# Kernel optimization log

Measured on AMD Instinct MI355X. Metric: run time of the kernel, lower is better.

The kernel has to match this reference:

```python
import jax, jax.numpy as jnp
import numpy as np

NUM_HEADS = 16
KEY_SIZE = 64
VALUE_SIZE = 64
D_MODEL = 1024
B, S = 2, 2048

def setup_inputs() -> dict:
    key = jax.random.key(0)
    k1, k2 = jax.random.split(key)
    inputs = jax.random.normal(k1, (B, S, D_MODEL), dtype=jnp.float32)
    qkv_width = NUM_HEADS * (KEY_SIZE + KEY_SIZE + VALUE_SIZE)  # 3072
    W = jax.random.normal(k2, (D_MODEL, qkv_width), dtype=jnp.float32) / np.sqrt(D_MODEL)
    b = jnp.zeros((qkv_width,), dtype=jnp.float32)
    return {"inputs": inputs, "W": W, "b": b}

def reference(inputs, W, b):
    # Fused QKV projection: [B, S, H*(2k+v)]
    qkv = jnp.einsum("bsd,de->bse", inputs, W) + b
    Bsz, S_ = inputs.shape[0], inputs.shape[1]
    qkv = qkv.reshape(Bsz, S_, NUM_HEADS, 2 * KEY_SIZE + VALUE_SIZE)
    qkv = jnp.transpose(qkv, (0, 2, 1, 3))  # [B, H, S, 2k+v]
    q = qkv[..., :KEY_SIZE]
    k = qkv[..., KEY_SIZE:2 * KEY_SIZE]
    v = qkv[..., 2 * KEY_SIZE:]
    # NOTE: original multiplies by sqrt(key_size) (not divide) -- faithful.
    scores = jnp.einsum("bhqd,bhkd->bhqk", q, k) * jnp.sqrt(jnp.float32(KEY_SIZE))
    weights = jax.nn.softmax(scores, axis=-1)
    out = jnp.einsum("bhqk,bhkv->bhqv", weights, v)  # [B, H, S, v]
    out = jnp.transpose(out, (0, 2, 1, 3)).reshape(Bsz, S_, NUM_HEADS * VALUE_SIZE)
    return out
```

## Files before the change

### kernel.cpp

```cpp
#include <hip/hip_runtime.h>


#define S_LEN 2048
#define NH    16
#define DH    64
#define DM    1024
#define EW    3072
#define NROWS 4096
#define NT    32

#define QSCALE 11.5415603f

using f32x4 = __attribute__((ext_vector_type(4))) float;
using bf8   = __attribute__((ext_vector_type(8))) short;
using s4v   = __attribute__((ext_vector_type(4))) short;

static __device__ __forceinline__ short f2bf(float f) {
  union { float f; unsigned u; } a; a.f = f;
  unsigned r = a.u + 0x7fffu + ((a.u >> 16) & 1u);
  return (short)(r >> 16);
}
static __device__ __forceinline__ float bf2f(short h) {
  union { float f; unsigned u; } a;
  a.u = ((unsigned)(unsigned short)h) << 16;
  return a.f;
}
static __device__ __forceinline__ void gl16(const void* g, void* l) {
  __builtin_amdgcn_global_load_lds(
      (const __attribute__((address_space(1))) void*)g,
      (__attribute__((address_space(3))) void*)l, 16, 0, 0);
}

__global__ __launch_bounds__(256) void prep(
    const float* __restrict__ X, const float* __restrict__ W,
    short* __restrict__ Xh, short* __restrict__ Xl,
    short* __restrict__ Wfh, short* __restrict__ Wfl) {
  __shared__ float t[32][33];
  const int id = blockIdx.x;
  if (id < 4096) {
    int i = id * 256 + threadIdx.x;
    float4 v = ((const float4*)X)[i];
    s4v h, l;
    h.x = f2bf(v.x); l.x = f2bf(v.x - bf2f(h.x));
    h.y = f2bf(v.y); l.y = f2bf(v.y - bf2f(h.y));
    h.z = f2bf(v.z); l.z = f2bf(v.z - bf2f(h.z));
    h.w = f2bf(v.w); l.w = f2bf(v.w - bf2f(h.w));
    ((s4v*)Xh)[i] = h;
    ((s4v*)Xl)[i] = l;
  } else {
    const int wid = id - 4096;
    int n0 = (wid % 96) * 32;
    int k0 = (wid / 96) * 32;
    int tx = threadIdx.x & 31;
    int ty = threadIdx.x >> 5;
#pragma unroll
    for (int i = 0; i < 32; i += 8)
      t[ty + i][tx] = W[(size_t)(k0 + ty + i) * EW + n0 + tx];
    __syncthreads();
    const int kt = k0 >> 5;
#pragma unroll
    for (int i = 0; i < 32; i += 8) {
      float v = t[tx][ty + i];
      int n = n0 + ty + i;
      int h = n / 192, e = n - h * 192;
      int np = (e < 64) ? (h * 64 + e)
             : (e < 128) ? (1024 + h * 64 + (e - 64))
                         : (2048 + h * 64 + (e - 128));
      int n16 = np >> 4, c = np & 15;
      int gg = (tx >> 3) & 3, ee = tx & 7;
      size_t o = ((size_t)(n16 * 32 + kt)) * 512 + (gg * 16 + c) * 8 + ee;
      short hi = f2bf(v);
      Wfh[o] = hi;
      if (np < 2048) Wfl[o] = f2bf(v - bf2f(hi));
    }
  }
}

__global__ __launch_bounds__(256, 2) void proj(
    const short* __restrict__ Xh, const short* __restrict__ Xl,
    const short* __restrict__ Wfh, const short* __restrict__ Wfl,
    const float* __restrict__ bias,
    short* __restrict__ Qh, short* __restrict__ Ql,
    short* __restrict__ Kh, short* __restrict__ Kl,
    short* __restrict__ Vt) {
  __shared__ short Ah[2][4096], Al[2][4096];
  const int tid = threadIdx.x;
  const int lane = tid & 63, w = tid >> 6;
  const int wr = w >> 1, wc = w & 1;
  const int c = lane & 15, g = lane >> 4;

  const int sr  = 32 * w + (lane >> 2);
  const int csw = ((lane & 3) ^ ((lane >> 3) & 3)) * 8;
  const int ldsw = w * 1024;
  const int rsw = (g ^ ((c >> 1) & 3)) * 8;

  if (blockIdx.x < 512) {
    const int id = blockIdx.x;
    const int t = id >> 3;
    const int rowBase = (((id & 7) << 2) + (t & 3)) * 128;
    const int colBase = (t >> 2) * 128;

    f32x4 acc[4][4] = {};
    const size_t aBase = (size_t)(rowBase + sr) * DM + csw;

    size_t bB[4];
#pragma unroll
    for (int n = 0; n < 4; ++n)
      bB[n] = ((size_t)((colBase >> 4) + wc * 4 + n) * 32) * 512 + lane * 8;

#define ASTAGE(B, kt) do {                                    \
    gl16(&Xh[aBase + (kt)],            &Ah[B][ldsw]);         \
    gl16(&Xh[aBase + (kt) + 16 * DM],  &Ah[B][ldsw + 512]);   \
    gl16(&Xl[aBase + (kt)],            &Al[B][ldsw]);         \
    gl16(&Xl[aBase + (kt) + 16 * DM],  &Al[B][ldsw + 512]);   \
  } while (0)
#define LOADB(dh, dl, kt) do {                                \
    _Pragma("unroll")                                         \
    for (int n = 0; n < 4; ++n) {                             \
      dh[n] = *(const bf8*)&Wfh[bB[n] + (size_t)(kt) * 512];  \
      dl[n] = *(const bf8*)&Wfl[bB[n] + (size_t)(kt) * 512];  \
    }                                                         \
  } while (0)
#define QKMFMA(bh, bl) do {                                   \
    _Pragma("unroll")                                         \
    for (int m = 0; m < 4; ++m) {                             \
      _Pragma("unroll")                                       \
      for (int n = 0; n < 4; ++n) {                           \
        acc[m][n] = __builtin_amdgcn_mfma_f32_16x16x32_bf16(al4[m], bh[n], acc[m][n], 0, 0, 0); \
        acc[m][n] = __builtin_amdgcn_mfma_f32_16x16x32_bf16(ah[m], bl[n], acc[m][n], 0, 0, 0);  \
        acc[m][n] = __builtin_amdgcn_mfma_f32_16x16x32_bf16(ah[m], bh[n], acc[m][n], 0, 0, 0);  \
      }                                                       \
    }                                                         \
  } while (0)

    bf8 b0h[4], b0l[4], b1h[4], b1l[4];
    LOADB(b0h, b0l, 0);
    ASTAGE(0, 0);
    __syncthreads();

    for (int it = 0; it < 32; it += 2) {
      LOADB(b1h, b1l, it + 1);
      bf8 ah[4], al4[4];
#pragma unroll
      for (int m = 0; m < 4; ++m) {
        int ro = (wr * 64 + m * 16 + c) * 32 + rsw;
        ah[m]  = *(const bf8*)&Ah[0][ro];
        al4[m] = *(const bf8*)&Al[0][ro];
      }
      ASTAGE(1, (it + 1) * 32);
      __builtin_amdgcn_s_setprio(1);
      QKMFMA(b0h, b0l);
      __builtin_amdgcn_s_setprio(0);
      __syncthreads();

      if (it + 2 < 32) LOADB(b0h, b0l, it + 2);
#pragma unroll
      for (int m = 0; m < 4; ++m) {
        int ro = (wr * 64 + m * 16 + c) * 32 + rsw;
        ah[m]  = *(const bf8*)&Ah[1][ro];
        al4[m] = *(const bf8*)&Al[1][ro];
      }
      if (it + 2 < 32) ASTAGE(0, (it + 2) * 32);
      __builtin_amdgcn_s_setprio(1);
      QKMFMA(b1h, b1l);
      __builtin_amdgcn_s_setprio(0);
      __syncthreads();
    }
#undef ASTAGE
#undef LOADB
#undef QKMFMA

#pragma unroll
    for (int m = 0; m < 4; ++m)
#pragma unroll
      for (int n = 0; n < 4; ++n)
#pragma unroll
        for (int j = 0; j < 4; ++j) {
          int grow = rowBase + wr * 64 + m * 16 + g * 4 + j;
          int gcol = colBase + wc * 64 + n * 16 + c;
          int h = (gcol >> 6) & 15, e = gcol & 63;
          int bb = grow >> 11, s = grow & 2047;
          size_t hb = (size_t)(bb * NH + h);
          if (gcol < 1024) {
            float q8 = (acc[m][n][j] + bias[h * 192 + e]) * QSCALE;
            short hi = f2bf(q8);
            short lo = f2bf(q8 - bf2f(hi));
            size_t idx = (hb * S_LEN + s) * DH + e;
            Qh[idx] = hi; Ql[idx] = lo;
          } else {
            float v = acc[m][n][j] + bias[h * 192 + 64 + e];
            short hi = f2bf(v);
            short lo = f2bf(v - bf2f(hi));
            int tile = s >> 6, r = s & 63;
            size_t idx = ((hb * NT + tile) * (size_t)4096) + r * 64 +
                         ((((e >> 3) ^ (r & 7)) << 3) | (e & 7));
            Kh[idx] = hi; Kl[idx] = lo;
          }
        }
  } else {
    const int id = blockIdx.x - 512;
    const int t = id >> 3;
    const int rowBase = (((id & 7) << 2) + (t & 3)) * 128;
    const int colBase = 2048 + (t >> 2) * 128;

    f32x4 acc[4][4] = {};
    const size_t aBase = (size_t)(rowBase + sr) * DM + csw;

    size_t bB[4];
#pragma unroll
    for (int n = 0; n < 4; ++n)
      bB[n] = ((size_t)((colBase >> 4) + wc * 4 + n) * 32) * 512 + lane * 8;

#define VASTAGE(B, kt) do {                                   \
    gl16(&Xh[aBase + (kt)],            &Ah[B][ldsw]);         \
    gl16(&Xh[aBase + (kt) + 16 * DM],  &Ah[B][ldsw + 512]);   \
  } while (0)
#define VLOADB(dh, kt) do {                                   \
    _Pragma("unroll")                                         \
    for (int n = 0; n < 4; ++n)                               \
      dh[n] = *(const bf8*)&Wfh[bB[n] + (size_t)(kt) * 512];  \
  } while (0)

    bf8 b0h[4], b1h[4];
    VLOADB(b0h, 0);
    VASTAGE(0, 0);
    __syncthreads();

    for (int it = 0; it < 32; it += 2) {
      VLOADB(b1h, it + 1);
      bf8 ah[4];
#pragma unroll
      for (int m = 0; m < 4; ++m)
        ah[m] = *(const bf8*)&Ah[0][(wr * 64 + m * 16 + c) * 32 + rsw];
      VASTAGE(1, (it + 1) * 32);
      __builtin_amdgcn_s_setprio(1);
#pragma unroll
      for (int m = 0; m < 4; ++m)
#pragma unroll
        for (int n = 0; n < 4; ++n)
          acc[m][n] = __builtin_amdgcn_mfma_f32_16x16x32_bf16(ah[m], b0h[n], acc[m][n], 0, 0, 0);
      __builtin_amdgcn_s_setprio(0);
      __syncthreads();

      if (it + 2 < 32) VLOADB(b0h, it + 2);
#pragma unroll
      for (int m = 0; m < 4; ++m)
        ah[m] = *(const bf8*)&Ah[1][(wr * 64 + m * 16 + c) * 32 + rsw];
      if (it + 2 < 32) VASTAGE(0, (it + 2) * 32);
      __builtin_amdgcn_s_setprio(1);
#pragma unroll
      for (int m = 0; m < 4; ++m)
#pragma unroll
        for (int n = 0; n < 4; ++n)
          acc[m][n] = __builtin_amdgcn_mfma_f32_16x16x32_bf16(ah[m], b1h[n], acc[m][n], 0, 0, 0);
      __builtin_amdgcn_s_setprio(0);
      __syncthreads();
    }
#undef VASTAGE
#undef VLOADB

#pragma unroll
    for (int m = 0; m < 4; ++m)
#pragma unroll
      for (int n = 0; n < 4; ++n)
#pragma unroll
        for (int j = 0; j < 4; ++j) {
          int grow = rowBase + wr * 64 + m * 16 + g * 4 + j;
          int gcol = colBase + wc * 64 + n * 16 + c;
          int h = (gcol >> 6) & 15, d = gcol & 63;
          int bb = grow >> 11, s = grow & 2047;
          size_t hb = (size_t)(bb * NH + h);
          float v = acc[m][n][j] + bias[h * 192 + 128 + d];
          int tile = s >> 6, key = s & 63;
          int kc = key >> 5, g4 = (key >> 2) & 3;
          int ii = (((key >> 4) & 1) << 2) | (key & 3);
          size_t idx = ((hb * NT + tile) * (size_t)4096) + d * 64 +
                       (((((kc << 2) | g4) ^ (d & 7)) << 3) | ii);
          Vt[idx] = f2bf(v);
        }
  }
}

__global__ __launch_bounds__(512, 4) void attn(
    const short* __restrict__ Qh, const short* __restrict__ Ql,
    const short* __restrict__ KhG, const short* __restrict__ KlG,
    const short* __restrict__ VtG, float* __restrict__ out) {
  __shared__ short KHs[2][4096];
  __shared__ short KLs[2][4096];
  __shared__ short Vs[2][4096];

  const int tid = threadIdx.x;
  const int lane = tid & 63, w = tid >> 6;
  const int c = lane & 15, g = lane >> 4;
  const int id = blockIdx.x;
  const int lid = (id & 7) * 64 + (id >> 3);
  const int bh = lid >> 4;
  const int q0 = (lid & 15) * 128 + w * 16;
  const size_t qBase  = (size_t)bh * S_LEN * DH;
  const size_t kvBase = (size_t)bh * NT * 4096;

  const int seg = tid * 8;

  bf8 qh[2], ql[2];
#pragma unroll
  for (int kc = 0; kc < 2; ++kc) {
    size_t idx = qBase + (size_t)(q0 + c) * DH + kc * 32 + g * 8;
    qh[kc] = *(const bf8*)&Qh[idx];
    ql[kc] = *(const bf8*)&Ql[idx];
  }

  int koff[2][4];
#pragma unroll
  for (int kc = 0; kc < 2; ++kc)
#pragma unroll
    for (int i = 0; i < 4; ++i)
      koff[kc][i] = (i * 16 + c) * 64 + (((kc * 4 + g) ^ (c & 7)) << 3);

  f32x4 mneg = {0.f, 0.f, 0.f, 0.f};
  f32x4 osum = {};
  f32x4 o[4] = {};
  union { bf8 v; unsigned u[4]; } ones;
  ones.u[0] = ones.u[1] = ones.u[2] = ones.u[3] = 0x3F803F80u;

  gl16(&KhG[kvBase + seg], &KHs[0][seg]);
  gl16(&KlG[kvBase + seg], &KLs[0][seg]);
  gl16(&VtG[kvBase + seg], &Vs[0][seg]);
  __syncthreads();

  for (int t = 0; t < NT; ++t) {
    const int cur = t & 1, nxt = cur ^ 1;
    if (t + 1 < NT) {
      size_t tb = kvBase + (size_t)(t + 1) * 4096 + seg;
      gl16(&KhG[tb], &KHs[nxt][seg]);
      gl16(&KlG[tb], &KLs[nxt][seg]);
      gl16(&VtG[tb], &Vs[nxt][seg]);
    }
    const short* KH = &KHs[cur][0];
    const short* KL = &KLs[cur][0];
    const short* VV = &Vs[cur][0];

    f32x4 sc[4];
    __builtin_amdgcn_s_setprio(1);
#pragma unroll
    for (int nb = 0; nb < 4; ++nb) {
      bf8 kh0 = *(const bf8*)&KH[koff[0][nb]];
      bf8 kl0 = *(const bf8*)&KL[koff[0][nb]];
      f32x4 s = __builtin_amdgcn_mfma_f32_16x16x32_bf16(kh0, ql[0], mneg, 0, 0, 0);
      s = __builtin_amdgcn_mfma_f32_16x16x32_bf16(kl0, qh[0], s, 0, 0, 0);
      s = __builtin_amdgcn_mfma_f32_16x16x32_bf16(kh0, qh[0], s, 0, 0, 0);
      bf8 kh1 = *(const bf8*)&KH[koff[1][nb]];
      bf8 kl1 = *(const bf8*)&KL[koff[1][nb]];
      s = __builtin_amdgcn_mfma_f32_16x16x32_bf16(kh1, ql[1], s, 0, 0, 0);
      s = __builtin_amdgcn_mfma_f32_16x16x32_bf16(kl1, qh[1], s, 0, 0, 0);
      s = __builtin_amdgcn_mfma_f32_16x16x32_bf16(kh1, qh[1], s, 0, 0, 0);
      sc[nb] = s;
    }
    __builtin_amdgcn_s_setprio(0);

    float m0 = fmaxf(fmaxf(sc[0][0], sc[0][1]), sc[0][2]);
    m0 = fmaxf(fmaxf(m0, sc[0][3]), sc[1][0]);
    m0 = fmaxf(fmaxf(m0, sc[1][1]), sc[1][2]);
    m0 = fmaxf(fmaxf(m0, sc[1][3]), sc[2][0]);
    m0 = fmaxf(fmaxf(m0, sc[2][1]), sc[2][2]);
    m0 = fmaxf(fmaxf(m0, sc[2][3]), sc[3][0]);
    m0 = fmaxf(fmaxf(m0, sc[3][1]), sc[3][2]);
    m0 = fmaxf(m0, sc[3][3]);
    m0 = fmaxf(m0, __shfl_xor(m0, 16));
    m0 = fmaxf(m0, __shfl_xor(m0, 32));

    if (__any(m0 > 8.0f)) {
      float delta = fmaxf(m0, 0.0f);
      float scale = exp2f(-delta);
      int sb = (g << 4) | (g << 2);
      float s0 = __shfl(scale, sb);
      float s1 = __shfl(scale, sb + 1);
      float s2 = __shfl(scale, sb + 2);
      float s3 = __shfl(scale, sb + 3);
#pragma unroll
      for (int db = 0; db < 4; ++db) {
        o[db][0] *= s0; o[db][1] *= s1; o[db][2] *= s2; o[db][3] *= s3;
      }
      osum[0] *= s0; osum[1] *= s1; osum[2] *= s2; osum[3] *= s3;
      mneg[0] -= delta; mneg[1] -= delta; mneg[2] -= delta; mneg[3] -= delta;
#pragma unroll
      for (int nb = 0; nb < 4; ++nb)
#pragma unroll
        for (int j = 0; j < 4; ++j)
          sc[nb][j] = exp2f(sc[nb][j] - delta);
    } else {
#pragma unroll
      for (int nb = 0; nb < 4; ++nb)
#pragma unroll
        for (int j = 0; j < 4; ++j)
          sc[nb][j] = exp2f(sc[nb][j]);
    }

    union { bf8 v; unsigned u[4]; } pa[2];
#pragma unroll
    for (int kc = 0; kc < 2; ++kc) {
      asm("v_cvt_pk_bf16_f32 %0, %1, %2"
          : "=v"(pa[kc].u[0]) : "v"(sc[2 * kc][0]), "v"(sc[2 * kc][1]));
      asm("v_cvt_pk_bf16_f32 %0, %1, %2"
          : "=v"(pa[kc].u[1]) : "v"(sc[2 * kc][2]), "v"(sc[2 * kc][3]));
      asm("v_cvt_pk_bf16_f32 %0, %1, %2"
          : "=v"(pa[kc].u[2]) : "v"(sc[2 * kc + 1][0]), "v"(sc[2 * kc + 1][1]));
      asm("v_cvt_pk_bf16_f32 %0, %1, %2"
          : "=v"(pa[kc].u[3]) : "v"(sc[2 * kc + 1][2]), "v"(sc[2 * kc + 1][3]));
    }

    __builtin_amdgcn_s_setprio(1);
#pragma unroll
    for (int kc = 0; kc < 2; ++kc) {
      osum = __builtin_amdgcn_mfma_f32_16x16x32_bf16(pa[kc].v, ones.v, osum, 0, 0, 0);
#pragma unroll
      for (int db = 0; db < 4; ++db) {
        bf8 vb = *(const bf8*)&VV[koff[kc][db]];
        o[db] = __builtin_amdgcn_mfma_f32_16x16x32_bf16(pa[kc].v, vb, o[db], 0, 0, 0);
      }
    }
    __builtin_amdgcn_s_setprio(0);

    __syncthreads();
  }

  float r0 = 1.f / osum[0];
  float r1 = 1.f / osum[1];
  float r2 = 1.f / osum[2];
  float r3 = 1.f / osum[3];

  const int b = bh >> 4, h = bh & 15;
#pragma unroll
  for (int db = 0; db < 4; ++db) {
    int col = h * DH + db * 16 + c;
    out[((size_t)b * S_LEN + q0 + g * 4 + 0) * DM + col] = o[db][0] * r0;
    out[((size_t)b * S_LEN + q0 + g * 4 + 1) * DM + col] = o[db][1] * r1;
    out[((size_t)b * S_LEN + q0 + g * 4 + 2) * DM + col] = o[db][2] * r2;
    out[((size_t)b * S_LEN + q0 + g * 4 + 3) * DM + col] = o[db][3] * r3;
  }
}

extern "C" void kernel_launch(void* const* d_in, const int* in_sizes, int n_in,
                              void* d_out, int out_size, void* d_ws, size_t ws_size,
                              hipStream_t stream) {
  const float* X    = (const float*)d_in[0];
  const float* W    = (const float*)d_in[1];
  const float* bias = (const float*)d_in[2];
  float* out = (float*)d_out;

  char* ws = (char*)d_ws;
  size_t off = 0;
  auto take = [&](size_t bytes) {
    void* p = ws + off;
    off += (bytes + 255) & ~(size_t)255;
    return p;
  };
  short* Xh  = (short*)take((size_t)NROWS * DM * 2);
  short* Xl  = (short*)take((size_t)NROWS * DM * 2);
  short* Wfh = (short*)take((size_t)EW * DM * 2);
  short* Wfl = (short*)take((size_t)EW * DM * 2);
  short* Qh  = (short*)take((size_t)2 * NH * S_LEN * DH * 2);
  short* Ql  = (short*)take((size_t)2 * NH * S_LEN * DH * 2);
  short* Kh  = (short*)take((size_t)2 * NH * NT * 4096 * 2);
  short* Kl  = (short*)take((size_t)2 * NH * NT * 4096 * 2);
  short* Vt  = (short*)take((size_t)2 * NH * NT * 4096 * 2);

  prep<<<dim3(4096 + 3072), dim3(256), 0, stream>>>(X, W, Xh, Xl, Wfh, Wfl);
  proj<<<dim3(768), dim3(256), 0, stream>>>(
      Xh, Xl, Wfh, Wfl, bias, Qh, Ql, Kh, Kl, Vt);
  attn<<<dim3(512), dim3(512), 0, stream>>>(
      Qh, Ql, Kh, Kl, Vt, out);
}
```

Before: 161.0 us.

## Remap proj warps to 128x32 column strips and raise occupancy to three blocks

Each of the four warps in the projection kernel now owns all 128 rows and a 32-column strip, where before it held a 64x64 quadrant. The warp keeps half as many B fragments in registers and loads the A fragments in two halves of four row-tiles each. Together with launch bounds raised to three blocks per CU, this is meant to cut register pressure so more waves can hide latency. In exchange each warp reads the full A tile from LDS, which doubles shared-memory read traffic per MFMA, and the software pipeline ordering is slightly changed.

```diff
diff --git a/kernel.cpp b/kernel.cpp
--- a/kernel.cpp
+++ b/kernel.cpp
@@ -76,7 +76,7 @@
   }
 }
 
-__global__ __launch_bounds__(256, 2) void proj(
+__global__ __launch_bounds__(256, 3) void proj(
     const short* __restrict__ Xh, const short* __restrict__ Xl,
     const short* __restrict__ Wfh, const short* __restrict__ Wfl,
     const float* __restrict__ bias,
@@ -86,7 +86,6 @@
   __shared__ short Ah[2][4096], Al[2][4096];
   const int tid = threadIdx.x;
   const int lane = tid & 63, w = tid >> 6;
-  const int wr = w >> 1, wc = w & 1;
   const int c = lane & 15, g = lane >> 4;
 
   const int sr  = 32 * w + (lane >> 2);
@@ -100,13 +99,13 @@
     const int rowBase = (((id & 7) << 2) + (t & 3)) * 128;
     const int colBase = (t >> 2) * 128;
 
-    f32x4 acc[4][4] = {};
+    f32x4 acc[8][2] = {};
     const size_t aBase = (size_t)(rowBase + sr) * DM + csw;
 
-    size_t bB[4];
-#pragma unroll
-    for (int n = 0; n < 4; ++n)
-      bB[n] = ((size_t)((colBase >> 4) + wc * 4 + n) * 32) * 512 + lane * 8;
+    size_t bB[2];
+#pragma unroll
+    for (int n = 0; n < 2; ++n)
+      bB[n] = ((size_t)((colBase >> 4) + w * 2 + n) * 32) * 512 + lane * 8;
 
 #define ASTAGE(B, kt) do {                                    \
     gl16(&Xh[aBase + (kt)],            &Ah[B][ldsw]);         \
@@ -116,68 +115,64 @@
   } while (0)
 #define LOADB(dh, dl, kt) do {                                \
     _Pragma("unroll")                                         \
-    for (int n = 0; n < 4; ++n) {                             \
+    for (int n = 0; n < 2; ++n) {                             \
       dh[n] = *(const bf8*)&Wfh[bB[n] + (size_t)(kt) * 512];  \
       dl[n] = *(const bf8*)&Wfl[bB[n] + (size_t)(kt) * 512];  \
     }                                                         \
   } while (0)
-#define QKMFMA(bh, bl) do {                                   \
-    _Pragma("unroll")                                         \
-    for (int m = 0; m < 4; ++m) {                             \
+#define QKHALF(B, h0, bh, bl) do {                            \
+    bf8 ah[4], al4[4];                                        \
+    _Pragma("unroll")                                         \
+    for (int mm = 0; mm < 4; ++mm) {                          \
+      int ro = (((h0) + mm) * 16 + c) * 32 + rsw;             \
+      ah[mm]  = *(const bf8*)&Ah[B][ro];                      \
+      al4[mm] = *(const bf8*)&Al[B][ro];                      \
+    }                                                         \
+    __builtin_amdgcn_s_setprio(1);                            \
+    _Pragma("unroll")                                         \
+    for (int mm = 0; mm < 4; ++mm) {                          \
       _Pragma("unroll")                                       \
-      for (int n = 0; n < 4; ++n) {                           \
-        acc[m][n] = __builtin_amdgcn_mfma_f32_16x16x32_bf16(al4[m], bh[n], acc[m][n], 0, 0, 0); \
-        acc[m][n] = __builtin_amdgcn_mfma_f32_16x16x32_bf16(ah[m], bl[n], acc[m][n], 0, 0, 0);  \
-        acc[m][n] = __builtin_amdgcn_mfma_f32_16x16x32_bf16(ah[m], bh[n], acc[m][n], 0, 0, 0);  \
+      for (int n = 0; n < 2; ++n) {                           \
+        acc[(h0) + mm][n] = __builtin_amdgcn_mfma_f32_16x16x32_bf16(al4[mm], bh[n], acc[(h0) + mm][n], 0, 0, 0); \
+        acc[(h0) + mm][n] = __builtin_amdgcn_mfma_f32_16x16x32_bf16(ah[mm], bl[n], acc[(h0) + mm][n], 0, 0, 0);  \
+        acc[(h0) + mm][n] = __builtin_amdgcn_mfma_f32_16x16x32_bf16(ah[mm], bh[n], acc[(h0) + mm][n], 0, 0, 0);  \
       }                                                       \
     }                                                         \
-  } while (0)
-
-    bf8 b0h[4], b0l[4], b1h[4], b1l[4];
+    __builtin_amdgcn_s_setprio(0);                            \
+  } while (0)
+
+    bf8 b0h[2], b0l[2], b1h[2], b1l[2];
     LOADB(b0h, b0l, 0);
     ASTAGE(0, 0);
     __syncthreads();
 
     for (int it = 0; it < 32; it += 2) {
       LOADB(b1h, b1l, it + 1);
-      bf8 ah[4], al4[4];
-#pragma unroll
-      for (int m = 0; m < 4; ++m) {
-        int ro = (wr * 64 + m * 16 + c) * 32 + rsw;
-        ah[m]  = *(const bf8*)&Ah[0][ro];
-        al4[m] = *(const bf8*)&Al[0][ro];
+      ASTAGE(1, (it + 1) * 32);
+      QKHALF(0, 0, b0h, b0l);
+      QKHALF(0, 4, b0h, b0l);
+      __syncthreads();
+
+      if (it + 2 < 32) {
+        LOADB(b0h, b0l, it + 2);
+        ASTAGE(0, (it + 2) * 32);
       }
-      ASTAGE(1, (it + 1) * 32);
-      __builtin_amdgcn_s_setprio(1);
-      QKMFMA(b0h, b0l);
-      __builtin_amdgcn_s_setprio(0);
-      __syncthreads();
-
-      if (it + 2 < 32) LOADB(b0h, b0l, it + 2);
-#pragma unroll
-      for (int m = 0; m < 4; ++m) {
-        int ro = (wr * 64 + m * 16 + c) * 32 + rsw;
-        ah[m]  = *(const bf8*)&Ah[1][ro];
-        al4[m] = *(const bf8*)&Al[1][ro];
-      }
-      if (it + 2 < 32) ASTAGE(0, (it + 2) * 32);
-      __builtin_amdgcn_s_setprio(1);
-      QKMFMA(b1h, b1l);
-      __builtin_amdgcn_s_setprio(0);
+      QKHALF(1, 0, b1h, b1l);
+      QKHALF(1, 4, b1h, b1l);
       __syncthreads();
     }
 #undef ASTAGE
 #undef LOADB
-#undef QKMFMA
-
-#pragma unroll
-    for (int m = 0; m < 4; ++m)
-#pragma unroll
-      for (int n = 0; n < 4; ++n)
+#undef QKHALF
+
+#pragma unroll
+    for (int m = 0; m < 8; ++m)
+#pragma unroll
+      for (int n = 0; n < 2; ++n)
 #pragma unroll
         for (int j = 0; j < 4; ++j) {
-          int grow = rowBase + wr * 64 + m * 16 + g * 4 + j;
-          int gcol = colBase + wc * 64 + n * 16 + c;
+          int grow = rowBase + m * 16 + g * 4 + j;
+          int gcol = colBase + w * 32 + n * 16 + c;
           int h = (gcol >> 6) & 15, e = gcol & 63;
           int bb = grow >> 11, s = grow & 2047;
           size_t hb = (size_t)(bb * NH + h);
@@ -203,13 +198,13 @@
     const int rowBase = (((id & 7) << 2) + (t & 3)) * 128;
     const int colBase = 2048 + (t >> 2) * 128;
 
-    f32x4 acc[4][4] = {};
+    f32x4 acc[8][2] = {};
     const size_t aBase = (size_t)(rowBase + sr) * DM + csw;
 
-    size_t bB[4];
-#pragma unroll
-    for (int n = 0; n < 4; ++n)
-      bB[n] = ((size_t)((colBase >> 4) + wc * 4 + n) * 32) * 512 + lane * 8;
+    size_t bB[2];
+#pragma unroll
+    for (int n = 0; n < 2; ++n)
+      bB[n] = ((size_t)((colBase >> 4) + w * 2 + n) * 32) * 512 + lane * 8;
 
 #define VASTAGE(B, kt) do {                                   \
     gl16(&Xh[aBase + (kt)],            &Ah[B][ldsw]);         \
@@ -217,56 +212,56 @@
   } while (0)
 #define VLOADB(dh, kt) do {                                   \
     _Pragma("unroll")                                         \
-    for (int n = 0; n < 4; ++n)                               \
+    for (int n = 0; n < 2; ++n)                               \
       dh[n] = *(const bf8*)&Wfh[bB[n] + (size_t)(kt) * 512];  \
   } while (0)
-
-    bf8 b0h[4], b1h[4];
+#define VHALF(B, h0, bh) do {                                 \
+    bf8 ah[4];                                                \
+    _Pragma("unroll")                                         \
+    for (int mm = 0; mm < 4; ++mm)                            \
+      ah[mm] = *(const bf8*)&Ah[B][(((h0) + mm) * 16 + c) * 32 + rsw]; \
+    __builtin_amdgcn_s_setprio(1);                            \
+    _Pragma("unroll")                                         \
+    for (int mm = 0; mm < 4; ++mm) {                          \
+      _Pragma("unroll")                                       \
+      for (int n = 0; n < 2; ++n)                             \
+        acc[(h0) + mm][n] = __builtin_amdgcn_mfma_f32_16x16x32_bf16(ah[mm], bh[n], acc[(h0) + mm][n], 0, 0, 0); \
+    }                                                         \
+    __builtin_amdgcn_s_setprio(0);                            \
+  } while (0)
+
+    bf8 b0h[2], b1h[2];
     VLOADB(b0h, 0);
     VASTAGE(0, 0);
     __syncthreads();
 
     for (int it = 0; it < 32; it += 2) {
       VLOADB(b1h, it + 1);
-      bf8 ah[4];
-#pragma unroll
-      for (int m = 0; m < 4; ++m)
-        ah[m] = *(const bf8*)&Ah[0][(wr * 64 + m * 16 + c) * 32 + rsw];
       VASTAGE(1, (it + 1) * 32);
-      __builtin_amdgcn_s_setprio(1);
-#pragma unroll
-      for (int m = 0; m < 4; ++m)
-#pragma unroll
-        for (int n = 0; n < 4; ++n)
-          acc[m][n] = __builtin_amdgcn_mfma_f32_16x16x32_bf16(ah[m], b0h[n], acc[m][n], 0, 0, 0);
-      __builtin_amdgcn_s_setprio(0);
+      VHALF(0, 0, b0h);
+      VHALF(0, 4, b0h);
       __syncthreads();
 
-      if (it + 2 < 32) VLOADB(b0h, it + 2);
-#pragma unroll
-      for (int m = 0; m < 4; ++m)
-        ah[m] = *(const bf8*)&Ah[1][(wr * 64 + m * 16 + c) * 32 + rsw];
-      if (it + 2 < 32) VASTAGE(0, (it + 2) * 32);
-      __builtin_amdgcn_s_setprio(1);
-#pragma unroll
-      for (int m = 0; m < 4; ++m)
-#pragma unroll
-        for (int n = 0; n < 4; ++n)
-          acc[m][n] = __builtin_amdgcn_mfma_f32_16x16x32_bf16(ah[m], b1h[n], acc[m][n], 0, 0, 0);
-      __builtin_amdgcn_s_setprio(0);
+      if (it + 2 < 32) {
+        VLOADB(b0h, it + 2);
+        VASTAGE(0, (it + 2) * 32);
+      }
+      VHALF(1, 0, b1h);
+      VHALF(1, 4, b1h);
       __syncthreads();
     }
 #undef VASTAGE
 #undef VLOADB
-
-#pragma unroll
-    for (int m = 0; m < 4; ++m)
-#pragma unroll
-      for (int n = 0; n < 4; ++n)
+#undef VHALF
+
+#pragma unroll
+    for (int m = 0; m < 8; ++m)
+#pragma unroll
+      for (int n = 0; n < 2; ++n)
 #pragma unroll
         for (int j = 0; j < 4; ++j) {
-          int grow = rowBase + wr * 64 + m * 16 + g * 4 + j;
-          int gcol = colBase + wc * 64 + n * 16 + c;
+          int grow = rowBase + m * 16 + g * 4 + j;
+          int gcol = colBase + w * 32 + n * 16 + c;
           int h = (gcol >> 6) & 15, d = gcol & 63;
           int bb = grow >> 11, s = grow & 2047;
           size_t hb = (size_t)(bb * NH + h);
```

After: 159.1 us, median of 2. Within noise of the previous version (-1.2%).
